# Optimization experiments

Hardware: AMD Instinct MI355X
Metric: run time of the kernel (lower is better)

The kernel has to match this reference:

```python
import jax, jax.numpy as jnp
import numpy as np

D_INNER, D_STATE, DT_RANK = 2048, 16, 128
BATCH, SEQ = 2, 2048


def setup_inputs() -> dict:
    key = jax.random.key(0)
    ks = jax.random.split(key, 6)
    x = jax.random.normal(ks[0], (BATCH, SEQ, D_INNER), dtype=jnp.float32)
    # A_log initialized uniform(-4, -1) per _init_parameters
    A_log = jax.random.uniform(ks[1], (D_INNER, D_STATE), minval=-4.0, maxval=-1.0, dtype=jnp.float32)
    D = jnp.ones((D_INNER,), dtype=jnp.float32)
    # torch Linear weights: [out_features, in_features], kaiming-uniform-ish scale
    x_proj_w = jax.random.normal(ks[2], (DT_RANK + 2 * D_STATE, D_INNER), dtype=jnp.float32) / np.sqrt(D_INNER)
    dt_proj_w = jax.random.normal(ks[3], (D_INNER, DT_RANK), dtype=jnp.float32) / np.sqrt(DT_RANK)
    dt_std = DT_RANK ** (-0.5)
    dt_proj_b = jax.random.uniform(ks[4], (D_INNER,), minval=-dt_std, maxval=dt_std, dtype=jnp.float32)
    return {"x": x, "A_log": A_log, "D": D, "x_proj_w": x_proj_w,
            "dt_proj_w": dt_proj_w, "dt_proj_b": dt_proj_b}


def _selective_scan(u, delta, A, B, C, D):
    # u, delta: [b, l, d]; A: [d, n]; B, C: [b, l, n]; D: [d]
    dA = jnp.exp(delta[..., None] * A[None, None])          # [b, l, d, n]
    dBu = (delta * u)[..., None] * B[:, :, None, :]         # [b, l, d, n]

    def step(h, inp):
        dA_t, dBu_t, C_t = inp                              # [b,d,n],[b,d,n],[b,n]
        h = dA_t * h + dBu_t
        y_t = jnp.einsum('bdn,bn->bd', h, C_t)
        return h, y_t

    h0 = jnp.zeros((u.shape[0], u.shape[2], A.shape[1]), dtype=u.dtype)
    xs = (jnp.moveaxis(dA, 1, 0), jnp.moveaxis(dBu, 1, 0), jnp.moveaxis(C, 1, 0))
    _, ys = jax.lax.scan(step, h0, xs)                      # ys: [l, b, d]
    y = jnp.moveaxis(ys, 0, 1)
    return y + u * D[None, None, :]


def reference(x, A_log, D, x_proj_w, dt_proj_w, dt_proj_b):
    # x: [b, l, d_inner]
    x_dbl = jnp.einsum('bld,ed->ble', x, x_proj_w)          # [b, l, dt_rank + 2n]
    delta_r = x_dbl[..., :DT_RANK]
    B = x_dbl[..., DT_RANK:DT_RANK + D_STATE]
    C = x_dbl[..., DT_RANK + D_STATE:]
    delta = jnp.einsum('blr,dr->bld', delta_r, dt_proj_w) + dt_proj_b
    delta = jax.nn.softplus(delta)                          # delta_softplus=True
    A = -jnp.exp(A_log)
    return _selective_scan(x, delta, A, B, C, D)
```

## Files before the change

kernel.cpp:

```cpp
#include <hip/hip_runtime.h>
#include <hip/hip_bf16.h>
#include <math.h>

#define DI   2048
#define DS   16
#define DTR  128
#define NBATCH 2
#define SEQ  2048
#define ROWS (NBATCH*SEQ)
#define NE   (DTR + 2*DS)
#define NC   64
#define LC   (SEQ/NC)

typedef float f32x4 __attribute__((ext_vector_type(4)));
typedef short s16x8 __attribute__((ext_vector_type(8)));
typedef short s16x4 __attribute__((ext_vector_type(4)));

#define L2E 1.4426950408889634f

__device__ inline short f2bf(float f) {
    unsigned u = __builtin_bit_cast(unsigned, f);
    u += 0x7FFFu + ((u >> 16) & 1u);
    return (short)(u >> 16);
}

__device__ inline unsigned pk2(float lo, float hi) {
    union { __hip_bfloat162 h; unsigned u; } cv;
    cv.h = __float22bfloat162_rn(float2{lo, hi});
    return cv.u;
}
__device__ inline unsigned packdu(short dbf, float xf) {
    return ((unsigned)(unsigned short)f2bf(xf) << 16) | (unsigned)(unsigned short)dbf;
}

__global__ __launch_bounds__(256) void k_castw(const float* __restrict__ w,
                                               const float* __restrict__ dtw,
                                               short* __restrict__ wb,
                                               short* __restrict__ dtwb) {
    int i = blockIdx.x*256 + threadIdx.x;
    if (i < 81920) {
        float4 v = ((const float4*)w)[i];
        s16x4 o = { f2bf(v.x), f2bf(v.y), f2bf(v.z), f2bf(v.w) };
        *(s16x4*)(wb + 4*i) = o;
    } else if (i < 147456) {
        int j = i - 81920;
        float4 v = ((const float4*)dtw)[j];
        s16x4 o = { f2bf(v.x), f2bf(v.y), f2bf(v.z), f2bf(v.w) };
        *(s16x4*)(dtwb + 4*j) = o;
    }
}

__global__ __launch_bounds__(512) void k_gemm1(const float* __restrict__ x,
                                               const short* __restrict__ wb,
                                               short* __restrict__ dRb,
                                               float* __restrict__ Bm,
                                               float* __restrict__ Cm) {
    __shared__ float lred[2][3][5][64][4];
    const int tid  = threadIdx.x;
    const int w    = tid >> 6;
    const int lane = tid & 63;
    const int half = w & 1, kq = w >> 1;
    const int m16  = blockIdx.x;
    const int r = lane & 15, g = lane >> 4;

    f32x4 acc[5] = {};
    const float* xp    = x  + (size_t)(m16*16 + r)*DI + g*8 + kq*512;
    const short* wbase = wb + (size_t)(half*80 + r)*DI + g*8 + kq*512;
    #pragma unroll 4
    for (int kk = 0; kk < 16; ++kk) {
        const int k0 = kk*32;
        float4 xa = *(const float4*)(xp + k0);
        float4 xc = *(const float4*)(xp + k0 + 4);
        union { s16x8 v; unsigned u[4]; } af;
        af.u[0] = pk2(xa.x, xa.y);
        af.u[1] = pk2(xa.z, xa.w);
        af.u[2] = pk2(xc.x, xc.y);
        af.u[3] = pk2(xc.z, xc.w);
        #pragma unroll
        for (int nf = 0; nf < 5; ++nf) {
            s16x8 bfrag = *(const s16x8*)(wbase + (size_t)nf*16*DI + k0);
            acc[nf] = __builtin_amdgcn_mfma_f32_16x16x32_bf16(af.v, bfrag, acc[nf], 0, 0, 0);
        }
    }
    if (kq > 0) {
        #pragma unroll
        for (int nf = 0; nf < 5; ++nf)
            *(f32x4*)&lred[half][kq-1][nf][lane][0] = acc[nf];
    }
    __syncthreads();
    if (kq == 0) {
        #pragma unroll
        for (int nf = 0; nf < 5; ++nf)
            #pragma unroll
            for (int p = 0; p < 3; ++p)
                acc[nf] += *(const f32x4*)&lred[half][p][nf][lane][0];
        const int orow = m16*16 + g*4;
        #pragma unroll
        for (int nf = 0; nf < 5; ++nf) {
            const int gnf = half*5 + nf;
            const int col = gnf*16 + r;
            #pragma unroll
            for (int j = 0; j < 4; ++j) {
                const int row = orow + j;
                float v = acc[nf][j];
                if (gnf < 8)       dRb[(size_t)row*DTR + col]        = f2bf(v);
                else if (gnf == 8) Bm [(size_t)row*DS + (col - 128)] = v;
                else               Cm [(size_t)row*DS + (col - 144)] = v;
            }
        }
    }
}

__global__ __launch_bounds__(256) void k_gemm2(const short* __restrict__ dRb,
                                               const short* __restrict__ dtwb,
                                               const float* __restrict__ bias,
                                               unsigned short* __restrict__ deltab) {
    const int wave = blockIdx.x*4 + (threadIdx.x >> 6);
    const int lane = threadIdx.x & 63;
    const int m16 = wave >> 5, nt = wave & 31;
    const int r = lane & 15, g = lane >> 4;

    s16x8 a[4];
    const short* ap = dRb + (size_t)(m16*16 + r)*DTR + g*8;
    #pragma unroll
    for (int ks = 0; ks < 4; ++ks) a[ks] = *(const s16x8*)(ap + ks*32);

    f32x4 acc[4] = {};
    #pragma unroll
    for (int nf = 0; nf < 4; ++nf) {
        const short* bp = dtwb + (size_t)(nt*64 + nf*16 + r)*DTR + g*8;
        #pragma unroll
        for (int ks = 0; ks < 4; ++ks) {
            s16x8 b = *(const s16x8*)(bp + ks*32);
            acc[nf] = __builtin_amdgcn_mfma_f32_16x16x32_bf16(a[ks], b, acc[nf], 0, 0, 0);
        }
    }
    const int orow = m16*16 + g*4;
    #pragma unroll
    for (int nf = 0; nf < 4; ++nf) {
        const int col = nt*64 + nf*16 + r;
        const float bb = bias[col];
        #pragma unroll
        for (int j = 0; j < 4; ++j) {
            float v = acc[nf][j] + bb;
            float sp = fmaxf(v, 0.f) + __logf(1.f + __expf(-fabsf(v)));
            deltab[(size_t)(orow + j)*DI + col] = (unsigned short)f2bf(sp);
        }
    }
}

__global__ __launch_bounds__(256) void k_scan1(const unsigned short* __restrict__ deltab,
                                               const float* __restrict__ x,
                                               const float* __restrict__ Bm,
                                               const float* __restrict__ A_log,
                                               float* __restrict__ aprod,
                                               float* __restrict__ rsum) {
    __shared__ unsigned lxd[LC][64];
    __shared__ float lB[LC][DS];
    const int tid = threadIdx.x;
    const int bb = blockIdx.x & 31;
    const int b  = (blockIdx.x >> 5) & 1;
    const int c  = blockIdx.x >> 6;
    const int d0 = bb*64;
    const int lbase = c*LC;

    {
        const unsigned short* dsrc = deltab + ((size_t)(b*SEQ + lbase))*DI + d0;
        const float*          xsrc = x      + ((size_t)(b*SEQ + lbase))*DI + d0;
        const int row = tid >> 4, col = (tid & 15)*4;
        #pragma unroll
        for (int i = 0; i < 2; i++) {
            s16x4  dv = *(const s16x4*) (dsrc + (size_t)(row + 16*i)*DI + col);
            float4 xv = *(const float4*)(xsrc + (size_t)(row + 16*i)*DI + col);
            uint4 o;
            o.x = packdu(dv[0], xv.x);
            o.y = packdu(dv[1], xv.y);
            o.z = packdu(dv[2], xv.z);
            o.w = packdu(dv[3], xv.w);
            *(uint4*)&lxd[row + 16*i][col] = o;
        }
        if (tid < 128) {
            const float* bsrc = Bm + ((size_t)(b*SEQ + lbase))*DS;
            *(float4*)&lB[tid >> 2][(tid & 3)*4] = *(const float4*)(bsrc + tid*4);
        }
    }

    const int lane = tid & 63, widx = tid >> 6;
    const int dlow = lane & 15, q = lane >> 4;
    const int dcol = widx*16 + dlow;
    const int d = d0 + dcol;
    const int n0 = 4*q;

    float4 Alg = *(const float4*)(A_log + (size_t)d*DS + n0);
    float An2[4] = { -__expf(Alg.x)*L2E, -__expf(Alg.y)*L2E,
                     -__expf(Alg.z)*L2E, -__expf(Alg.w)*L2E };
    float r[4] = {0.f,0.f,0.f,0.f};
    float S = 0.f;

    __syncthreads();

    #pragma unroll 8
    for (int tt = 0; tt < LC; ++tt) {
        unsigned v = lxd[tt][dcol];
        float dlt = __builtin_bit_cast(float, v << 16);
        float u   = __builtin_bit_cast(float, v & 0xffff0000u);
        float du  = dlt * u;
        S += dlt;
        float4 bv = *(const float4*)&lB[tt][n0];
        float bbv[4] = {bv.x, bv.y, bv.z, bv.w};
        #pragma unroll
        for (int j = 0; j < 4; ++j) {
            float da = exp2f(An2[j] * dlt);
            r[j] = fmaf(da, r[j], du * bbv[j]);
        }
    }
    size_t base = (((size_t)c*NBATCH + b)*DI + d)*DS + n0;
    *(f32x4*)(aprod + base) = (f32x4){ exp2f(An2[0]*S), exp2f(An2[1]*S),
                                       exp2f(An2[2]*S), exp2f(An2[3]*S) };
    *(f32x4*)(rsum  + base) = (f32x4){ r[0], r[1], r[2], r[3] };
}

__global__ __launch_bounds__(256) void k_mid(float* __restrict__ ah,
                                             const float* __restrict__ rsum) {
    __shared__ float lA[8][32];
    __shared__ float lR[8][32];
    const int tid = threadIdx.x;
    const int s  = tid >> 5;
    const int el = tid & 31;
    const size_t E = (size_t)NBATCH*DI*DS;
    const size_t e = (size_t)blockIdx.x*32 + el;

    float a[8], r[8];
    #pragma unroll
    for (int i = 0; i < 8; ++i) {
        size_t idx = (size_t)(s*8 + i)*E + e;
        a[i] = ah[idx];
        r[i] = rsum[idx];
    }
    float A = 1.f, R = 0.f;
    #pragma unroll
    for (int i = 0; i < 8; ++i) {
        A = a[i]*A;
        R = fmaf(a[i], R, r[i]);
    }
    lA[s][el] = A; lR[s][el] = R;
    __syncthreads();
    float h = 0.f;
    for (int k = 0; k < s; ++k)
        h = fmaf(lA[k][el], h, lR[k][el]);
    #pragma unroll
    for (int i = 0; i < 8; ++i) {
        size_t idx = (size_t)(s*8 + i)*E + e;
        ah[idx] = h;
        h = fmaf(a[i], h, r[i]);
    }
}

__global__ __launch_bounds__(256) void k_scan2(const unsigned short* __restrict__ deltab,
                                               const float* __restrict__ x,
                                               const float* __restrict__ Bm,
                                               const float* __restrict__ Cm,
                                               const float* __restrict__ A_log,
                                               const float* __restrict__ Dv,
                                               const float* __restrict__ hin,
                                               float* __restrict__ y) {
    __shared__ unsigned lxd[LC][64];
    __shared__ float lB[LC][DS];
    __shared__ float lC[LC][DS];
    const int tid = threadIdx.x;
    const int bb = blockIdx.x & 31;
    const int b  = (blockIdx.x >> 5) & 1;
    const int c  = blockIdx.x >> 6;
    const int d0 = bb*64;
    const int lbase = c*LC;

    {
        const unsigned short* dsrc = deltab + ((size_t)(b*SEQ + lbase))*DI + d0;
        const float*          xsrc = x      + ((size_t)(b*SEQ + lbase))*DI + d0;
        const int row = tid >> 4, col = (tid & 15)*4;
        #pragma unroll
        for (int i = 0; i < 2; i++) {
            s16x4  dv = *(const s16x4*) (dsrc + (size_t)(row + 16*i)*DI + col);
            float4 xv = *(const float4*)(xsrc + (size_t)(row + 16*i)*DI + col);
            uint4 o;
            o.x = packdu(dv[0], xv.x);
            o.y = packdu(dv[1], xv.y);
            o.z = packdu(dv[2], xv.z);
            o.w = packdu(dv[3], xv.w);
            *(uint4*)&lxd[row + 16*i][col] = o;
        }
        if (tid < 128) {
            const float* bsrc = Bm + ((size_t)(b*SEQ + lbase))*DS;
            const float* csrc = Cm + ((size_t)(b*SEQ + lbase))*DS;
            *(float4*)&lB[tid >> 2][(tid & 3)*4] = *(const float4*)(bsrc + tid*4);
            *(float4*)&lC[tid >> 2][(tid & 3)*4] = *(const float4*)(csrc + tid*4);
        }
    }

    const int lane = tid & 63, widx = tid >> 6;
    const int dlow = lane & 15, q = lane >> 4;
    const int dcol = widx*16 + dlow;
    const int d = d0 + dcol;
    const int n0 = 4*q;

    float4 Alg = *(const float4*)(A_log + (size_t)d*DS + n0);
    float An2[4] = { -__expf(Alg.x)*L2E, -__expf(Alg.y)*L2E,
                     -__expf(Alg.z)*L2E, -__expf(Alg.w)*L2E };
    size_t base = (((size_t)c*NBATCH + b)*DI + d)*DS + n0;
    float4 hv = *(const float4*)(hin + base);
    float h[4] = {hv.x, hv.y, hv.z, hv.w};
    const float Dd = Dv[d];
    float* yp = y + ((size_t)(b*SEQ + lbase))*DI + d;

    __syncthreads();

    #pragma unroll 8
    for (int tt = 0; tt < LC; ++tt) {
        unsigned v = lxd[tt][dcol];
        float dlt = __builtin_bit_cast(float, v << 16);
        float u   = __builtin_bit_cast(float, v & 0xffff0000u);
        float du  = dlt * u;
        float4 bv = *(const float4*)&lB[tt][n0];
        float4 cv = *(const float4*)&lC[tt][n0];
        float bbv[4] = {bv.x, bv.y, bv.z, bv.w};
        float ccv[4] = {cv.x, cv.y, cv.z, cv.w};
        float acc = 0.f;
        #pragma unroll
        for (int j = 0; j < 4; ++j) {
            float da = exp2f(An2[j] * dlt);
            h[j] = fmaf(da, h[j], du * bbv[j]);
            acc  = fmaf(h[j], ccv[j], acc);
        }
        acc += __shfl_xor(acc, 16);
        acc += __shfl_xor(acc, 32);
        if (q == 0) yp[(size_t)tt*DI] = fmaf(u, Dd, acc);
    }
}

extern "C" void kernel_launch(void* const* d_in, const int* in_sizes, int n_in,
                              void* d_out, int out_size, void* d_ws, size_t ws_size,
                              hipStream_t stream) {
    const float* x     = (const float*)d_in[0];
    const float* A_log = (const float*)d_in[1];
    const float* Dv    = (const float*)d_in[2];
    const float* xpw   = (const float*)d_in[3];
    const float* dtw   = (const float*)d_in[4];
    const float* dtb   = (const float*)d_in[5];
    float* out = (float*)d_out;

    const size_t SCN = (size_t)NC*NBATCH*DS*DI;

    float* ws    = (float*)d_ws;
    unsigned short* deltab = (unsigned short*)ws;
    float* aprod = ws + ((size_t)ROWS*DI/2);
    float* rsum  = aprod + SCN;
    float* Bm    = rsum + SCN;
    float* Cm    = Bm + (size_t)ROWS*DS;
    short* dRb   = (short*)(Cm + (size_t)ROWS*DS);
    short* wb    = dRb + (size_t)ROWS*DTR;
    short* dtwb  = wb  + (size_t)160*2048;

    k_castw<<<576, 256, 0, stream>>>(xpw, dtw, wb, dtwb);
    k_gemm1<<<256, 512, 0, stream>>>(x, wb, dRb, Bm, Cm);
    k_gemm2<<<2048, 256, 0, stream>>>(dRb, dtwb, dtb, deltab);
    k_scan1<<<4096, 256, 0, stream>>>(deltab, x, Bm, A_log, aprod, rsum);
    k_mid<<<2048, 256, 0, stream>>>(aprod, rsum);
    k_scan2<<<4096, 256, 0, stream>>>(deltab, x, Bm, Cm, A_log, Dv, aprod, out);
}
```

Before: 230.3 us.

## Halve scan chunk count, give each thread two channels, use native exp2

```diff
diff --git a/kernel.cpp b/kernel.cpp
--- a/kernel.cpp
+++ b/kernel.cpp
@@ -9,7 +9,7 @@
 #define SEQ  2048
 #define ROWS (NBATCH*SEQ)
 #define NE   (DTR + 2*DS)
-#define NC   64
+#define NC   32
 #define LC   (SEQ/NC)
 
 typedef float f32x4 __attribute__((ext_vector_type(4)));
@@ -17,6 +17,12 @@
 typedef short s16x4 __attribute__((ext_vector_type(4)));
 
 #define L2E 1.4426950408889634f
+
+#if __has_builtin(__builtin_amdgcn_exp2f)
+#define EXP2(v) __builtin_amdgcn_exp2f(v)
+#else
+#define EXP2(v) __expf((v)*0.6931471805599453f)
+#endif
 
 __device__ inline short f2bf(float f) {
     unsigned u = __builtin_bit_cast(unsigned, f);
@@ -155,69 +161,78 @@
                                                const float* __restrict__ A_log,
                                                float* __restrict__ aprod,
                                                float* __restrict__ rsum) {
-    __shared__ unsigned lxd[LC][64];
+    __shared__ unsigned lxd[LC][128];
     __shared__ float lB[LC][DS];
     const int tid = threadIdx.x;
-    const int bb = blockIdx.x & 31;
-    const int b  = (blockIdx.x >> 5) & 1;
-    const int c  = blockIdx.x >> 6;
-    const int d0 = bb*64;
+    const int bb = blockIdx.x & 15;
+    const int b  = (blockIdx.x >> 4) & 1;
+    const int c  = blockIdx.x >> 5;
+    const int d0 = bb*128;
     const int lbase = c*LC;
 
     {
         const unsigned short* dsrc = deltab + ((size_t)(b*SEQ + lbase))*DI + d0;
         const float*          xsrc = x      + ((size_t)(b*SEQ + lbase))*DI + d0;
-        const int row = tid >> 4, col = (tid & 15)*4;
-        #pragma unroll
-        for (int i = 0; i < 2; i++) {
-            s16x4  dv = *(const s16x4*) (dsrc + (size_t)(row + 16*i)*DI + col);
-            float4 xv = *(const float4*)(xsrc + (size_t)(row + 16*i)*DI + col);
+        const int srow = tid >> 5, scol = (tid & 31)*4;
+        #pragma unroll
+        for (int i = 0; i < 8; i++) {
+            int rr = srow + 8*i;
+            s16x4  dv = *(const s16x4*) (dsrc + (size_t)rr*DI + scol);
+            float4 xv = *(const float4*)(xsrc + (size_t)rr*DI + scol);
             uint4 o;
             o.x = packdu(dv[0], xv.x);
             o.y = packdu(dv[1], xv.y);
             o.z = packdu(dv[2], xv.z);
             o.w = packdu(dv[3], xv.w);
-            *(uint4*)&lxd[row + 16*i][col] = o;
-        }
-        if (tid < 128) {
-            const float* bsrc = Bm + ((size_t)(b*SEQ + lbase))*DS;
-            *(float4*)&lB[tid >> 2][(tid & 3)*4] = *(const float4*)(bsrc + tid*4);
-        }
+            *(uint4*)&lxd[rr][scol] = o;
+        }
+        const float* bsrc = Bm + ((size_t)(b*SEQ + lbase))*DS;
+        *(float4*)&lB[tid >> 2][(tid & 3)*4] = *(const float4*)(bsrc + tid*4);
     }
 
     const int lane = tid & 63, widx = tid >> 6;
     const int dlow = lane & 15, q = lane >> 4;
-    const int dcol = widx*16 + dlow;
-    const int d = d0 + dcol;
+    const int ca = widx*32 + dlow, cb = ca + 16;
+    const int dA = d0 + ca, dB = d0 + cb;
     const int n0 = 4*q;
 
-    float4 Alg = *(const float4*)(A_log + (size_t)d*DS + n0);
-    float An2[4] = { -__expf(Alg.x)*L2E, -__expf(Alg.y)*L2E,
-                     -__expf(Alg.z)*L2E, -__expf(Alg.w)*L2E };
-    float r[4] = {0.f,0.f,0.f,0.f};
-    float S = 0.f;
+    float4 AlgA = *(const float4*)(A_log + (size_t)dA*DS + n0);
+    float4 AlgB = *(const float4*)(A_log + (size_t)dB*DS + n0);
+    float An2[8] = { -__expf(AlgA.x)*L2E, -__expf(AlgA.y)*L2E,
+                     -__expf(AlgA.z)*L2E, -__expf(AlgA.w)*L2E,
+                     -__expf(AlgB.x)*L2E, -__expf(AlgB.y)*L2E,
+                     -__expf(AlgB.z)*L2E, -__expf(AlgB.w)*L2E };
+    float r0[4] = {0.f,0.f,0.f,0.f}, r1[4] = {0.f,0.f,0.f,0.f};
+    float S0 = 0.f, S1 = 0.f;
 
     __syncthreads();
 
-    #pragma unroll 8
+    #pragma unroll 4
     for (int tt = 0; tt < LC; ++tt) {
-        unsigned v = lxd[tt][dcol];
-        float dlt = __builtin_bit_cast(float, v << 16);
-        float u   = __builtin_bit_cast(float, v & 0xffff0000u);
-        float du  = dlt * u;
-        S += dlt;
+        unsigned va = lxd[tt][ca];
+        unsigned vb = lxd[tt][cb];
+        float dltA = __builtin_bit_cast(float, va << 16);
+        float uA   = __builtin_bit_cast(float, va & 0xffff0000u);
+        float dltB = __builtin_bit_cast(float, vb << 16);
+        float uB   = __builtin_bit_cast(float, vb & 0xffff0000u);
+        float duA = dltA * uA, duB = dltB * uB;
+        S0 += dltA; S1 += dltB;
         float4 bv = *(const float4*)&lB[tt][n0];
         float bbv[4] = {bv.x, bv.y, bv.z, bv.w};
         #pragma unroll
         for (int j = 0; j < 4; ++j) {
-            float da = exp2f(An2[j] * dlt);
-            r[j] = fmaf(da, r[j], du * bbv[j]);
-        }
-    }
-    size_t base = (((size_t)c*NBATCH + b)*DI + d)*DS + n0;
-    *(f32x4*)(aprod + base) = (f32x4){ exp2f(An2[0]*S), exp2f(An2[1]*S),
-                                       exp2f(An2[2]*S), exp2f(An2[3]*S) };
-    *(f32x4*)(rsum  + base) = (f32x4){ r[0], r[1], r[2], r[3] };
+            r0[j] = fmaf(EXP2(An2[j]   * dltA), r0[j], duA * bbv[j]);
+            r1[j] = fmaf(EXP2(An2[j+4] * dltB), r1[j], duB * bbv[j]);
+        }
+    }
+    size_t baseA = (((size_t)c*NBATCH + b)*DI + dA)*DS + n0;
+    size_t baseB = (((size_t)c*NBATCH + b)*DI + dB)*DS + n0;
+    *(f32x4*)(aprod + baseA) = (f32x4){ EXP2(An2[0]*S0), EXP2(An2[1]*S0),
+                                        EXP2(An2[2]*S0), EXP2(An2[3]*S0) };
+    *(f32x4*)(aprod + baseB) = (f32x4){ EXP2(An2[4]*S1), EXP2(An2[5]*S1),
+                                        EXP2(An2[6]*S1), EXP2(An2[7]*S1) };
+    *(f32x4*)(rsum + baseA) = (f32x4){ r0[0], r0[1], r0[2], r0[3] };
+    *(f32x4*)(rsum + baseB) = (f32x4){ r1[0], r1[1], r1[2], r1[3] };
 }
 
 __global__ __launch_bounds__(256) void k_mid(float* __restrict__ ah,
@@ -230,16 +245,16 @@
     const size_t E = (size_t)NBATCH*DI*DS;
     const size_t e = (size_t)blockIdx.x*32 + el;
 
-    float a[8], r[8];
-    #pragma unroll
-    for (int i = 0; i < 8; ++i) {
-        size_t idx = (size_t)(s*8 + i)*E + e;
+    float a[4], r[4];
+    #pragma unroll
+    for (int i = 0; i < 4; ++i) {
+        size_t idx = (size_t)(s*4 + i)*E + e;
         a[i] = ah[idx];
         r[i] = rsum[idx];
     }
     float A = 1.f, R = 0.f;
     #pragma unroll
-    for (int i = 0; i < 8; ++i) {
+    for (int i = 0; i < 4; ++i) {
         A = a[i]*A;
         R = fmaf(a[i], R, r[i]);
     }
@@ -249,8 +264,8 @@
     for (int k = 0; k < s; ++k)
         h = fmaf(lA[k][el], h, lR[k][el]);
     #pragma unroll
-    for (int i = 0; i < 8; ++i) {
-        size_t idx = (size_t)(s*8 + i)*E + e;
+    for (int i = 0; i < 4; ++i) {
+        size_t idx = (size_t)(s*4 + i)*E + e;
         ah[idx] = h;
         h = fmaf(a[i], h, r[i]);
     }
@@ -264,76 +279,90 @@
                                                const float* __restrict__ Dv,
                                                const float* __restrict__ hin,
                                                float* __restrict__ y) {
-    __shared__ unsigned lxd[LC][64];
+    __shared__ unsigned lxd[LC][128];
     __shared__ float lB[LC][DS];
     __shared__ float lC[LC][DS];
     const int tid = threadIdx.x;
-    const int bb = blockIdx.x & 31;
-    const int b  = (blockIdx.x >> 5) & 1;
-    const int c  = blockIdx.x >> 6;
-    const int d0 = bb*64;
+    const int bb = blockIdx.x & 15;
+    const int b  = (blockIdx.x >> 4) & 1;
+    const int c  = blockIdx.x >> 5;
+    const int d0 = bb*128;
     const int lbase = c*LC;
 
     {
         const unsigned short* dsrc = deltab + ((size_t)(b*SEQ + lbase))*DI + d0;
         const float*          xsrc = x      + ((size_t)(b*SEQ + lbase))*DI + d0;
-        const int row = tid >> 4, col = (tid & 15)*4;
-        #pragma unroll
-        for (int i = 0; i < 2; i++) {
-            s16x4  dv = *(const s16x4*) (dsrc + (size_t)(row + 16*i)*DI + col);
-            float4 xv = *(const float4*)(xsrc + (size_t)(row + 16*i)*DI + col);
+        const int srow = tid >> 5, scol = (tid & 31)*4;
+        #pragma unroll
+        for (int i = 0; i < 8; i++) {
+            int rr = srow + 8*i;
+            s16x4  dv = *(const s16x4*) (dsrc + (size_t)rr*DI + scol);
+            float4 xv = *(const float4*)(xsrc + (size_t)rr*DI + scol);
             uint4 o;
             o.x = packdu(dv[0], xv.x);
             o.y = packdu(dv[1], xv.y);
             o.z = packdu(dv[2], xv.z);
             o.w = packdu(dv[3], xv.w);
-            *(uint4*)&lxd[row + 16*i][col] = o;
-        }
-        if (tid < 128) {
-            const float* bsrc = Bm + ((size_t)(b*SEQ + lbase))*DS;
-            const float* csrc = Cm + ((size_t)(b*SEQ + lbase))*DS;
-            *(float4*)&lB[tid >> 2][(tid & 3)*4] = *(const float4*)(bsrc + tid*4);
-            *(float4*)&lC[tid >> 2][(tid & 3)*4] = *(const float4*)(csrc + tid*4);
-        }
+            *(uint4*)&lxd[rr][scol] = o;
+        }
+        const float* bsrc = Bm + ((size_t)(b*SEQ + lbase))*DS;
+        const float* csrc = Cm + ((size_t)(b*SEQ + lbase))*DS;
+        *(float4*)&lB[tid >> 2][(tid & 3)*4] = *(const float4*)(bsrc + tid*4);
+        *(float4*)&lC[tid >> 2][(tid & 3)*4] = *(const float4*)(csrc + tid*4);
     }
 
     const int lane = tid & 63, widx = tid >> 6;
     const int dlow = lane & 15, q = lane >> 4;
-    const int dcol = widx*16 + dlow;
-    const int d = d0 + dcol;
+    const int ca = widx*32 + dlow, cb = ca + 16;
+    const int dA = d0 + ca, dB = d0 + cb;
     const int n0 = 4*q;
 
-    float4 Alg = *(const float4*)(A_log + (size_t)d*DS + n0);
-    float An2[4] = { -__expf(Alg.x)*L2E, -__expf(Alg.y)*L2E,
-                     -__expf(Alg.z)*L2E, -__expf(Alg.w)*L2E };
-    size_t base = (((size_t)c*NBATCH + b)*DI + d)*DS + n0;
-    float4 hv = *(const float4*)(hin + base);
-    float h[4] = {hv.x, hv.y, hv.z, hv.w};
-    const float Dd = Dv[d];
-    float* yp = y + ((size_t)(b*SEQ + lbase))*DI + d;
+    float4 AlgA = *(const float4*)(A_log + (size_t)dA*DS + n0);
+    float4 AlgB = *(const float4*)(A_log + (size_t)dB*DS + n0);
+    float An2[8] = { -__expf(AlgA.x)*L2E, -__expf(AlgA.y)*L2E,
+                     -__expf(AlgA.z)*L2E, -__expf(AlgA.w)*L2E,
+                     -__expf(AlgB.x)*L2E, -__expf(AlgB.y)*L2E,
+                     -__expf(AlgB.z)*L2E, -__expf(AlgB.w)*L2E };
+    size_t baseA = (((size_t)c*NBATCH + b)*DI + dA)*DS + n0;
+    size_t baseB = (((size_t)c*NBATCH + b)*DI + dB)*DS + n0;
+    float4 hvA = *(const float4*)(hin + baseA);
+    float4 hvB = *(const float4*)(hin + baseB);
+    float h0[4] = {hvA.x, hvA.y, hvA.z, hvA.w};
+    float h1[4] = {hvB.x, hvB.y, hvB.z, hvB.w};
+    const float DdA = Dv[dA], DdB = Dv[dB];
+    float* yp = y + ((size_t)(b*SEQ + lbase))*DI + d0;
 
     __syncthreads();
 
-    #pragma unroll 8
+    #pragma unroll 4
     for (int tt = 0; tt < LC; ++tt) {
-        unsigned v = lxd[tt][dcol];
-        float dlt = __builtin_bit_cast(float, v << 16);
-        float u   = __builtin_bit_cast(float, v & 0xffff0000u);
-        float du  = dlt * u;
+        unsigned va = lxd[tt][ca];
+        unsigned vb = lxd[tt][cb];
+        float dltA = __builtin_bit_cast(float, va << 16);
+        float uA   = __builtin_bit_cast(float, va & 0xffff0000u);
+        float dltB = __builtin_bit_cast(float, vb << 16);
+        float uB   = __builtin_bit_cast(float, vb & 0xffff0000u);
+        float duA = dltA * uA, duB = dltB * uB;
         float4 bv = *(const float4*)&lB[tt][n0];
         float4 cv = *(const float4*)&lC[tt][n0];
         float bbv[4] = {bv.x, bv.y, bv.z, bv.w};
         float ccv[4] = {cv.x, cv.y, cv.z, cv.w};
-        float acc = 0.f;
+        float accA = 0.f, accB = 0.f;
         #pragma unroll
         for (int j = 0; j < 4; ++j) {
-            float da = exp2f(An2[j] * dlt);
-            h[j] = fmaf(da, h[j], du * bbv[j]);
-            acc  = fmaf(h[j], ccv[j], acc);
-        }
-        acc += __shfl_xor(acc, 16);
-        acc += __shfl_xor(acc, 32);
-        if (q == 0) yp[(size_t)tt*DI] = fmaf(u, Dd, acc);
+            h0[j] = fmaf(EXP2(An2[j]   * dltA), h0[j], duA * bbv[j]);
+            h1[j] = fmaf(EXP2(An2[j+4] * dltB), h1[j], duB * bbv[j]);
+            accA  = fmaf(h0[j], ccv[j], accA);
+            accB  = fmaf(h1[j], ccv[j], accB);
+        }
+        accA += __shfl_xor(accA, 16);
+        accA += __shfl_xor(accA, 32);
+        accB += __shfl_xor(accB, 16);
+        accB += __shfl_xor(accB, 32);
+        if (q == 0) {
+            yp[(size_t)tt*DI + ca] = fmaf(uA, DdA, accA);
+            yp[(size_t)tt*DI + cb] = fmaf(uB, DdB, accB);
+        }
     }
 }
 
@@ -363,7 +392,7 @@
     k_castw<<<576, 256, 0, stream>>>(xpw, dtw, wb, dtwb);
     k_gemm1<<<256, 512, 0, stream>>>(x, wb, dRb, Bm, Cm);
     k_gemm2<<<2048, 256, 0, stream>>>(dRb, dtwb, dtb, deltab);
-    k_scan1<<<4096, 256, 0, stream>>>(deltab, x, Bm, A_log, aprod, rsum);
+    k_scan1<<<1024, 256, 0, stream>>>(deltab, x, Bm, A_log, aprod, rsum);
     k_mid<<<2048, 256, 0, stream>>>(aprod, rsum);
-    k_scan2<<<4096, 256, 0, stream>>>(deltab, x, Bm, Cm, A_log, Dv, aprod, out);
-}
+    k_scan2<<<1024, 256, 0, stream>>>(deltab, x, Bm, Cm, A_log, Dv, aprod, out);
+}
```

New measurement: 208.7 us. -9.4%, faster.
